# Performance work log

Measured on AMD Instinct MI355X. Metric: run time of the kernel, lower is better.

Reference implementation:

```python
import jax, jax.numpy as jnp
import numpy as np

N_NODES = 50000
N_EDGES = 1600000
DIM_IN = 128
DIM_OUT = 128
EPS = 1e-10


def setup_inputs() -> dict:
    key = jax.random.key(0)
    k1, k2, k3, k4, k5 = jax.random.split(key, 5)
    feat_in = jax.random.normal(k1, (N_NODES, DIM_IN), dtype=jnp.float32)
    rows = jax.random.randint(k2, (N_EDGES,), 0, N_NODES, dtype=jnp.int32)
    cols = jax.random.randint(k3, (N_EDGES,), 0, N_NODES, dtype=jnp.int32)
    # normalized adjacency values (positive, ~1/deg scale)
    vals = jax.random.uniform(k4, (N_EDGES,), dtype=jnp.float32) / 32.0
    W = jax.random.normal(k5, (DIM_OUT, DIM_IN), dtype=jnp.float32) * 0.05
    b = jnp.zeros((DIM_OUT,), dtype=jnp.float32)
    scale = jnp.ones((DIM_OUT,), dtype=jnp.float32)
    offset = jnp.zeros((DIM_OUT,), dtype=jnp.float32)
    return {"feat_in": feat_in, "rows": rows, "cols": cols, "vals": vals,
            "W": W, "b": b, "scale": scale, "offset": offset}


def reference(feat_in, rows, cols, vals, W, b, scale, offset):
    # torch.sparse.mm(adj_norm, feat_in): gather source features, scale by
    # edge value, scatter-add into destination rows.
    msgs = vals[:, None] * feat_in[cols]                       # [E, D_in]
    feat_aggr = jax.ops.segment_sum(msgs, rows, num_segments=N_NODES)  # [N, D_in]
    # f_lin (nn.Linear): x @ W.T + b
    feat_trans = feat_aggr @ W.T + b                           # [N, D_out]
    # act = ReLU
    a = jax.nn.relu(feat_trans)
    # f_norm: per-row (feature-dim) normalization, biased variance
    mean = jnp.mean(a, axis=1, keepdims=True)
    var = jnp.mean((a - mean) ** 2, axis=1, keepdims=True) + EPS
    feat_out = (a - mean) * scale * jax.lax.rsqrt(var) + offset
    return feat_out
```

## Files before the change

kernel.cpp:

```cpp
#include <hip/hip_runtime.h>

typedef unsigned int uint;
typedef unsigned short ushort;
typedef __attribute__((ext_vector_type(8))) short short8;
typedef __attribute__((ext_vector_type(4))) float floatx4;

#define N_NODES 50000
#define N_EDGES 1600000
#define DIM 128
#define LN_EPS 1e-10f

#define NB2 1564
#define CAP2 1280
#define EPB 6250
#define SB 256
#define CAPR 76

__device__ __forceinline__ uint f2bf(float x) {
    uint u = __float_as_uint(x);
    return (u + 0x7FFFu + ((u >> 16) & 1u)) >> 16;
}

__global__ __launch_bounds__(256) void setup(
    const float* __restrict__ feat, const float* __restrict__ W,
    uint* __restrict__ featb_u, ushort* __restrict__ wbf,
    int* __restrict__ gcnt)
{
    const int stride = gridDim.x * 256;
    if (blockIdx.x == 0)
        for (int i = threadIdx.x; i < NB2; i += 256) gcnt[i] = 0;
    for (int i = blockIdx.x * 256 + threadIdx.x; i < N_NODES * DIM / 4; i += stride) {
        float4 v = ((const float4*)feat)[i];
        ((uint2*)featb_u)[i] = make_uint2(
            f2bf(v.x) | (f2bf(v.y) << 16),
            f2bf(v.z) | (f2bf(v.w) << 16));
    }
    for (int i = blockIdx.x * 256 + threadIdx.x; i < DIM * DIM / 4; i += stride) {
        float4 v = ((const float4*)W)[i];
        ushort4 o;
        o.x = (ushort)f2bf(v.x); o.y = (ushort)f2bf(v.y);
        o.z = (ushort)f2bf(v.z); o.w = (ushort)f2bf(v.w);
        ((ushort4*)wbf)[i] = o;
    }
}

__global__ __launch_bounds__(1024) void scatter(
    const int* __restrict__ rows, const int* __restrict__ cols,
    const float* __restrict__ vals, int* __restrict__ gcnt,
    int2* __restrict__ perm)
{
    __shared__ int  cnt[NB2];
    __shared__ int  gbase[NB2];
    __shared__ int  lbase[NB2];
    __shared__ int  csum[64];
    __shared__ int2 stageE[EPB];
    const int bx = blockIdx.x;
    const int t  = threadIdx.x;

    for (int i = t; i < NB2; i += 1024) cnt[i] = 0;
    __syncthreads();
    const int base = bx * EPB;
    uint pk[7];
    #pragma unroll
    for (int i = 0; i < 7; ++i) {
        int k = i * 1024 + t;
        if (k < EPB) {
            int r = rows[base + k];
            int rank = atomicAdd(&cnt[r >> 5], 1);
            pk[i] = ((uint)rank << 16) | (uint)r;
        }
    }
    __syncthreads();

    for (int i = t; i < NB2; i += 1024) {
        int c = cnt[i];
        gbase[i] = c ? atomicAdd(&gcnt[i], c) : 0;
    }
    if (t < 64) {
        int s = 0;
        for (int j = 0; j < 25; ++j) {
            int idx = t * 25 + j;
            if (idx < NB2) s += cnt[idx];
        }
        csum[t] = s;
    }
    __syncthreads();
    if (t == 0) {
        int s = 0;
        for (int i = 0; i < 64; ++i) { int c = csum[i]; csum[i] = s; s += c; }
    }
    __syncthreads();
    if (t < 64) {
        int run = csum[t];
        for (int j = 0; j < 25; ++j) {
            int idx = t * 25 + j;
            if (idx < NB2) { lbase[idx] = run; run += cnt[idx]; }
        }
    }
    __syncthreads();

    #pragma unroll
    for (int i = 0; i < 7; ++i) {
        int k = i * 1024 + t;
        if (k < EPB) {
            uint s = pk[i];
            int r = (int)(s & 0xFFFFu);
            int rank = (int)(s >> 16);
            int b = r >> 5;
            int pos = lbase[b] + rank;
            stageE[pos] = make_int2(
                (uint)cols[base + k] | ((uint)(r & 31) << 16) | ((uint)b << 21),
                __float_as_int(vals[base + k]));
        }
    }
    __syncthreads();

    for (int j = t; j < EPB; j += 1024) {
        int2 p = stageE[j];
        uint b = ((uint)p.x) >> 21;
        int pos = gbase[b] + (j - lbase[b]);
        if (pos < CAP2)
            perm[(size_t)b * CAP2 + pos] = p;
    }
}

__global__ __launch_bounds__(512, 8) void agg_fused(
    const int2* __restrict__ perm, const int* __restrict__ gcnt,
    const ushort* __restrict__ featb, const ushort* __restrict__ wbf,
    const float* __restrict__ bias, const float* __restrict__ scale,
    const float* __restrict__ offset, float* __restrict__ out)
{
    __shared__ int2 lists[32 * CAPR];
    ushort* rowsbuf = (ushort*)lists;
    float*  Cbuf    = (float*)lists;
    __shared__ int  lcnt[32];

    const int t = threadIdx.x;

    const int q = NB2 >> 3, rr = NB2 & 7;
    const int xcd = blockIdx.x & 7, within = blockIdx.x >> 3;
    const int hb = (xcd < rr ? xcd * (q + 1) : rr * (q + 1) + (xcd - rr) * q) + within;

    if (t < 32) lcnt[t] = 0;
    __syncthreads();

    int n = gcnt[hb];
    if (n > CAP2) n = CAP2;
    const int2* pb = perm + (size_t)hb * CAP2;

    for (int e = t; e < n; e += 512) {
        int2 p = pb[e];
        int rl = (p.x >> 16) & 31;
        int pos = atomicAdd(&lcnt[rl], 1);
        if (pos < CAPR)
            lists[rl * CAPR + pos] = make_int2((p.x & 0xFFFF) << 8, p.y);
    }
    __syncthreads();

    const int lane = t & 63;
    const int wid  = t >> 6;
    const int rb   = wid * 4;
    const char* fbase = (const char*)featb;
    const uint  lane4 = (uint)lane << 2;

    float ax[4], ay[4];
    #pragma unroll
    for (int j = 0; j < 4; ++j) {
        int rl = rb + j;
        int cnt = lcnt[rl];
        if (cnt > CAPR) cnt = CAPR;
        const int2* L = &lists[rl * CAPR];
        float sx = 0.f, sy = 0.f;
        int e = 0;
        for (; e + 11 < cnt; e += 12) {
            int4 q6[6]; uint g[12];
            #pragma unroll
            for (int k = 0; k < 6; ++k) q6[k] = *(const int4*)&L[e + 2 * k];
            #pragma unroll
            for (int k = 0; k < 6; ++k) {
                g[2*k]   = *(const uint*)(fbase + ((uint)q6[k].x + lane4));
                g[2*k+1] = *(const uint*)(fbase + ((uint)q6[k].z + lane4));
            }
            #pragma unroll
            for (int k = 0; k < 6; ++k) {
                float v0 = __int_as_float(q6[k].y);
                float v1 = __int_as_float(q6[k].w);
                sx = fmaf(v0, __uint_as_float(g[2*k] << 16), sx);
                sy = fmaf(v0, __uint_as_float(g[2*k] & 0xFFFF0000u), sy);
                sx = fmaf(v1, __uint_as_float(g[2*k+1] << 16), sx);
                sy = fmaf(v1, __uint_as_float(g[2*k+1] & 0xFFFF0000u), sy);
            }
        }
        for (; e + 3 < cnt; e += 4) {
            int4 q2[2]; uint g[4];
            #pragma unroll
            for (int k = 0; k < 2; ++k) q2[k] = *(const int4*)&L[e + 2 * k];
            #pragma unroll
            for (int k = 0; k < 2; ++k) {
                g[2*k]   = *(const uint*)(fbase + ((uint)q2[k].x + lane4));
                g[2*k+1] = *(const uint*)(fbase + ((uint)q2[k].z + lane4));
            }
            #pragma unroll
            for (int k = 0; k < 2; ++k) {
                float v0 = __int_as_float(q2[k].y);
                float v1 = __int_as_float(q2[k].w);
                sx = fmaf(v0, __uint_as_float(g[2*k] << 16), sx);
                sy = fmaf(v0, __uint_as_float(g[2*k] & 0xFFFF0000u), sy);
                sx = fmaf(v1, __uint_as_float(g[2*k+1] << 16), sx);
                sy = fmaf(v1, __uint_as_float(g[2*k+1] & 0xFFFF0000u), sy);
            }
        }
        for (; e < cnt; ++e) {
            int2 p = L[e];
            uint g = *(const uint*)(fbase + ((uint)p.x + lane4));
            float v = __int_as_float(p.y);
            sx = fmaf(v, __uint_as_float(g << 16), sx);
            sy = fmaf(v, __uint_as_float(g & 0xFFFF0000u), sy);
        }
        ax[j] = sx; ay[j] = sy;
    }
    __syncthreads();

    #pragma unroll
    for (int j = 0; j < 4; ++j) {
        uint pk = f2bf(ax[j]) | (f2bf(ay[j]) << 16);
        *(uint*)&rowsbuf[(rb + j) * 136 + 2 * lane] = pk;
    }
    __syncthreads();

    const int l15  = lane & 15;
    const int quad = lane >> 4;
    const int n0   = wid * 16 + l15;
    const float bb = bias[n0];

    floatx4 acc0 = {0.f, 0.f, 0.f, 0.f};
    floatx4 acc1 = {0.f, 0.f, 0.f, 0.f};
    #pragma unroll
    for (int kt = 0; kt < 4; ++kt) {
        int k0 = kt * 32 + quad * 8;
        short8 af0 = *(const short8*)&rowsbuf[l15 * 136 + k0];
        short8 af1 = *(const short8*)&rowsbuf[(l15 + 16) * 136 + k0];
        short8 bf  = *(const short8*)&wbf[n0 * DIM + k0];
        acc0 = __builtin_amdgcn_mfma_f32_16x16x32_bf16(af0, bf, acc0, 0, 0, 0);
        acc1 = __builtin_amdgcn_mfma_f32_16x16x32_bf16(af1, bf, acc1, 0, 0, 0);
    }
    __syncthreads();

    #pragma unroll
    for (int r = 0; r < 4; ++r) {
        int m = quad * 4 + r;
        Cbuf[m * 132 + n0]        = acc0[r] + bb;
        Cbuf[(m + 16) * 132 + n0] = acc1[r] + bb;
    }
    __syncthreads();

    const float sc0 = scale[lane],  sc1 = scale[lane + 64];
    const float of0 = offset[lane], of1 = offset[lane + 64];

    #pragma unroll
    for (int j = 0; j < 4; ++j) {
        int rl = rb + j;
        int r  = hb * 32 + rl;
        if (r >= N_NODES) continue;
        float A0 = fmaxf(Cbuf[rl * 132 + lane],      0.0f);
        float A1 = fmaxf(Cbuf[rl * 132 + lane + 64], 0.0f);

        float s = A0 + A1;
        #pragma unroll
        for (int off = 32; off >= 1; off >>= 1) s += __shfl_xor(s, off, 64);
        float mean = s * (1.0f / 128.0f);

        float d0 = A0 - mean, d1 = A1 - mean;
        float q2 = d0 * d0 + d1 * d1;
        #pragma unroll
        for (int off = 32; off >= 1; off >>= 1) q2 += __shfl_xor(q2, off, 64);
        float rstd = rsqrtf(q2 * (1.0f / 128.0f) + LN_EPS);

        size_t rowp = (size_t)r * DIM;
        out[rowp + lane]      = d0 * sc0 * rstd + of0;
        out[rowp + lane + 64] = d1 * sc1 * rstd + of1;
    }
}

extern "C" void kernel_launch(void* const* d_in, const int* in_sizes, int n_in,
                              void* d_out, int out_size, void* d_ws, size_t ws_size,
                              hipStream_t stream) {
    const float* feat_in = (const float*)d_in[0];
    const int*   rows    = (const int*)d_in[1];
    const int*   cols    = (const int*)d_in[2];
    const float* vals    = (const float*)d_in[3];
    const float* W       = (const float*)d_in[4];
    const float* bias    = (const float*)d_in[5];
    const float* scale   = (const float*)d_in[6];
    const float* offset  = (const float*)d_in[7];
    float* out = (float*)d_out;

    char* p = (char*)d_ws;
    int2* perm = (int2*)p;                 p += (size_t)NB2 * CAP2 * 8;
    ushort* featb = (ushort*)p;            p += (size_t)N_NODES * DIM * 2;
    ushort* wbf = (ushort*)p;              p += DIM * DIM * 2;
    int*  gcnt = (int*)p;                  p += (size_t)(NB2 + 64) * 4;

    setup<<<1024, 256, 0, stream>>>(feat_in, W, (uint*)featb, wbf, gcnt);
    scatter<<<SB, 1024, 0, stream>>>(rows, cols, vals, gcnt, perm);
    agg_fused<<<NB2, 512, 0, stream>>>(perm, gcnt, featb, wbf,
                                       bias, scale, offset, out);
}
```

Baseline: 174.9 us.

## Merge bf16 conversion into scatter launch and rotate global counter atomics

The separate setup kernel is removed. Feature and weight bf16 conversion now runs in extra blocks of the scatter launch, so conversion overlaps with edge bucketing, and the counter zeroing moves to a memset. Each scatter block also starts its global atomicAdd loop at a block-dependent rotated offset to spread contention across bucket counters. This saves a kernel launch boundary. The cost is that conversion blocks take 1024-thread slots with large static LDS that they never use, which may limit concurrency.

Result: faster. 170.7 us (-2.4%).

```diff
diff --git a/kernel.cpp b/kernel.cpp
--- a/kernel.cpp
+++ b/kernel.cpp
@@ -14,6 +14,7 @@
 #define CAP2 1280
 #define EPB 6250
 #define SB 256
+#define CONVB 256
 #define CAPR 76
 
 __device__ __forceinline__ uint f2bf(float x) {
@@ -21,33 +22,12 @@
     return (u + 0x7FFFu + ((u >> 16) & 1u)) >> 16;
 }
 
-__global__ __launch_bounds__(256) void setup(
+__global__ __launch_bounds__(1024, 8) void prep(
     const float* __restrict__ feat, const float* __restrict__ W,
-    uint* __restrict__ featb_u, ushort* __restrict__ wbf,
-    int* __restrict__ gcnt)
-{
-    const int stride = gridDim.x * 256;
-    if (blockIdx.x == 0)
-        for (int i = threadIdx.x; i < NB2; i += 256) gcnt[i] = 0;
-    for (int i = blockIdx.x * 256 + threadIdx.x; i < N_NODES * DIM / 4; i += stride) {
-        float4 v = ((const float4*)feat)[i];
-        ((uint2*)featb_u)[i] = make_uint2(
-            f2bf(v.x) | (f2bf(v.y) << 16),
-            f2bf(v.z) | (f2bf(v.w) << 16));
-    }
-    for (int i = blockIdx.x * 256 + threadIdx.x; i < DIM * DIM / 4; i += stride) {
-        float4 v = ((const float4*)W)[i];
-        ushort4 o;
-        o.x = (ushort)f2bf(v.x); o.y = (ushort)f2bf(v.y);
-        o.z = (ushort)f2bf(v.z); o.w = (ushort)f2bf(v.w);
-        ((ushort4*)wbf)[i] = o;
-    }
-}
-
-__global__ __launch_bounds__(1024) void scatter(
     const int* __restrict__ rows, const int* __restrict__ cols,
     const float* __restrict__ vals, int* __restrict__ gcnt,
-    int2* __restrict__ perm)
+    int2* __restrict__ perm, uint* __restrict__ featb_u,
+    ushort* __restrict__ wbf)
 {
     __shared__ int  cnt[NB2];
     __shared__ int  gbase[NB2];
@@ -57,6 +37,25 @@
     const int bx = blockIdx.x;
     const int t  = threadIdx.x;
 
+    if (bx >= SB) {
+        const int cb = bx - SB;
+        const int stride = CONVB * 1024;
+        for (int i = cb * 1024 + t; i < N_NODES * DIM / 4; i += stride) {
+            float4 v = ((const float4*)feat)[i];
+            ((uint2*)featb_u)[i] = make_uint2(
+                f2bf(v.x) | (f2bf(v.y) << 16),
+                f2bf(v.z) | (f2bf(v.w) << 16));
+        }
+        for (int i = cb * 1024 + t; i < DIM * DIM / 4; i += stride) {
+            float4 v = ((const float4*)W)[i];
+            ushort4 o;
+            o.x = (ushort)f2bf(v.x); o.y = (ushort)f2bf(v.y);
+            o.z = (ushort)f2bf(v.z); o.w = (ushort)f2bf(v.w);
+            ((ushort4*)wbf)[i] = o;
+        }
+        return;
+    }
+
     for (int i = t; i < NB2; i += 1024) cnt[i] = 0;
     __syncthreads();
     const int base = bx * EPB;
@@ -72,9 +71,13 @@
     }
     __syncthreads();
 
-    for (int i = t; i < NB2; i += 1024) {
-        int c = cnt[i];
-        gbase[i] = c ? atomicAdd(&gcnt[i], c) : 0;
+    {
+        const int rot = (bx * 16) % NB2;
+        for (int i = t; i < NB2; i += 1024) {
+            int ii = i + rot; if (ii >= NB2) ii -= NB2;
+            int c = cnt[ii];
+            gbase[ii] = c ? atomicAdd(&gcnt[ii], c) : 0;
+        }
     }
     if (t < 64) {
         int s = 0;
@@ -301,8 +304,10 @@
     ushort* wbf = (ushort*)p;              p += DIM * DIM * 2;
     int*  gcnt = (int*)p;                  p += (size_t)(NB2 + 64) * 4;
 
-    setup<<<1024, 256, 0, stream>>>(feat_in, W, (uint*)featb, wbf, gcnt);
-    scatter<<<SB, 1024, 0, stream>>>(rows, cols, vals, gcnt, perm);
+    hipMemsetAsync(gcnt, 0, (size_t)NB2 * sizeof(int), stream);
+
+    prep<<<SB + CONVB, 1024, 0, stream>>>(feat_in, W, rows, cols, vals,
+                                          gcnt, perm, (uint*)featb, wbf);
     agg_fused<<<NB2, 512, 0, stream>>>(perm, gcnt, featb, wbf,
                                        bias, scale, offset, out);
 }
```
